# Kernel optimization log

Measured on AMD Instinct MI355X. Metric: run time of the kernel, lower is better.

The kernel has to match this reference:

```python
import jax, jax.numpy as jnp
import numpy as np

N, E = 100000, 1600000
HID, N_CHUNKS, STRU = 128, 8, 4


def setup_inputs() -> dict:
    key = jax.random.key(0)
    ks = jax.random.split(key, 7)
    x = jax.random.normal(ks[0], (N, HID), dtype=jnp.float32)
    e = jax.random.randint(ks[1], (2, E), 0, N, dtype=jnp.int64)
    ratio = jax.random.uniform(ks[2], (), dtype=jnp.float32)
    out_w = N_CHUNKS * STRU
    Wq = jax.random.normal(ks[3], (out_w, HID), dtype=jnp.float32) / np.sqrt(HID)
    bq = jax.random.normal(ks[4], (out_w,), dtype=jnp.float32) * 0.01
    Wv = jax.random.normal(ks[5], (out_w, HID), dtype=jnp.float32) / np.sqrt(HID)
    bv = jax.random.normal(ks[6], (out_w,), dtype=jnp.float32) * 0.01
    return {"x": x, "e": e, "ratio": ratio, "Wq": Wq, "bq": bq, "Wv": Wv, "bv": bv}


def reference(x, e, ratio, Wq, bq, Wv, bv):
    # edge-indexed gather of endpoint features: [E, HID]
    eu = x[e[0]]
    ev = x[e[1]]
    # two linear projections, elementwise multiply: [E, STRU*N_CHUNKS]
    ku = eu @ Wq.T + bq
    kv = ev @ Wv.T + bv
    ks = ku * kv
    # hsplit(STRU) -> STRU contiguous chunks of width N_CHUNKS; sum each chunk
    sums = ks.reshape(E, STRU, N_CHUNKS).sum(axis=-1)  # [E, STRU]
    w = jax.nn.sigmoid(sums) * (1.0 - ratio) * 0.5 + 1.0
    # original returns a list of STRU arrays of shape [E]; stack for a single output
    return jnp.transpose(w)  # [STRU, E]
```

## Files before the change

kernel.cpp:

```cpp
#include <hip/hip_runtime.h>
#include <hip/hip_bf16.h>
#include <cstddef>

constexpr int HID  = 128;
constexpr int OUTW = 32;
constexpr int TOT  = 64;
constexpr int STRU = 4;
constexpr int NCH  = 8;

typedef short  bf16x8 __attribute__((ext_vector_type(8)));
typedef float  f32x4  __attribute__((ext_vector_type(4)));
typedef int    int4v  __attribute__((ext_vector_type(4)));
typedef unsigned short u16x8 __attribute__((ext_vector_type(8)));

__device__ __forceinline__ unsigned short f2bf(float f) {
    unsigned u = __builtin_bit_cast(unsigned, f);
    u += 0x7FFFu + ((u >> 16) & 1u);
    return (unsigned short)(u >> 16);
}

__device__ __forceinline__ float dot4(float4 a, float4 b) {
    return a.x * b.x + a.y * b.y + a.z * b.z + a.w * b.w;
}

__device__ __forceinline__ float bfdot(int4v a, int4v b, float sum) {
#pragma unroll
    for (int w = 0; w < 4; ++w) {
        float alo = __builtin_bit_cast(float, (unsigned)(a[w] << 16));
        float ahi = __builtin_bit_cast(float, (unsigned)a[w] & 0xffff0000u);
        float blo = __builtin_bit_cast(float, (unsigned)(b[w] << 16));
        float bhi = __builtin_bit_cast(float, (unsigned)b[w] & 0xffff0000u);
        sum = fmaf(alo, blo, sum);
        sum = fmaf(ahi, bhi, sum);
    }
    return sum;
}

__global__ __launch_bounds__(256) void prep_bf16(
    const float* __restrict__ Wq, const float* __restrict__ bq,
    const float* __restrict__ Wv, const float* __restrict__ bv,
    unsigned short* __restrict__ Wfrag, float* __restrict__ bias)
{
    int tid = blockIdx.x * blockDim.x + threadIdx.x;
    if (tid < TOT * HID) {
        int j    = tid & 7;
        int lane = (tid >> 3) & 63;
        int kc   = (tid >> 9) & 3;
        int t    = tid >> 11;
        int o = t * 16 + (lane & 15);
        int k = kc * 32 + (lane >> 4) * 8 + j;
        float w = (o < OUTW) ? Wq[o * HID + k] : Wv[(o - OUTW) * HID + k];
        Wfrag[tid] = f2bf(w);
    }
    if (tid < TOT) bias[tid] = (tid < OUTW) ? bq[tid] : bv[tid - OUTW];
}

__global__ __launch_bounds__(256) void proj_mfma(
    const float* __restrict__ x,
    const unsigned short* __restrict__ Wfrag,
    const float* __restrict__ bias,
    unsigned short* __restrict__ P,
    unsigned short* __restrict__ Q,
    int n_nodes)
{
    __shared__ unsigned short sW[16 * 64 * 8];
    __shared__ unsigned short sPQ[64][TOT + 8];

    const int tid  = threadIdx.x;
    const int wid  = tid >> 6;
    const int lane = tid & 63;
    const int lr   = lane & 15;
    const int lg   = lane >> 4;
    const int base = blockIdx.x * 64;
    const int m0   = base + wid * 16;

    const int  arow = m0 + lr;
    const bool aok  = arow < n_nodes;
    const float* ap = x + (size_t)arow * HID;

    f32x4 xv[8];
#pragma unroll
    for (int kc = 0; kc < 4; ++kc) {
        if (aok) {
            const f32x4* p = reinterpret_cast<const f32x4*>(ap + kc * 32 + lg * 8);
            xv[2 * kc + 0] = p[0];
            xv[2 * kc + 1] = p[1];
        } else {
            xv[2 * kc + 0] = (f32x4)0.f;
            xv[2 * kc + 1] = (f32x4)0.f;
        }
    }

    {
        const int4v* src = reinterpret_cast<const int4v*>(Wfrag);
        int4v*       dst = reinterpret_cast<int4v*>(sW);
#pragma unroll
        for (int j = 0; j < 4; ++j)
            dst[tid + 256 * j] = src[tid + 256 * j];
    }

    f32x4 acc[4];
#pragma unroll
    for (int t = 0; t < 4; ++t) {
        float b = bias[t * 16 + lr];
        acc[t][0] = b; acc[t][1] = b; acc[t][2] = b; acc[t][3] = b;
    }

    __syncthreads();

#pragma unroll
    for (int kc = 0; kc < 4; ++kc) {
        f32x4 f0 = xv[2 * kc + 0], f1 = xv[2 * kc + 1];
        bf16x8 a;
        a[0] = (short)f2bf(f0[0]); a[1] = (short)f2bf(f0[1]);
        a[2] = (short)f2bf(f0[2]); a[3] = (short)f2bf(f0[3]);
        a[4] = (short)f2bf(f1[0]); a[5] = (short)f2bf(f1[1]);
        a[6] = (short)f2bf(f1[2]); a[7] = (short)f2bf(f1[3]);
#pragma unroll
        for (int t = 0; t < 4; ++t) {
            bf16x8 bf = *reinterpret_cast<const bf16x8*>(sW + ((size_t)(t * 4 + kc) * 64 + lane) * 8);
            acc[t] = __builtin_amdgcn_mfma_f32_16x16x32_bf16(a, bf, acc[t], 0, 0, 0);
        }
    }

    const int lrow = wid * 16 + lg * 4;
#pragma unroll
    for (int t = 0; t < 4; ++t)
#pragma unroll
        for (int j = 0; j < 4; ++j)
            sPQ[lrow + j][t * 16 + lr] = f2bf(acc[t][j]);
    __syncthreads();

    const int row  = tid >> 2;
    const int q    = tid & 3;
    const int node = base + row;
    if (node < n_nodes) {
        const int scol = q * 16;
        u16x8 v0 = *reinterpret_cast<const u16x8*>(&sPQ[row][scol]);
        u16x8 v1 = *reinterpret_cast<const u16x8*>(&sPQ[row][scol + 8]);
        unsigned short* dstbase = (q < 2) ? (P + (size_t)node * OUTW + q * 16)
                                          : (Q + (size_t)node * OUTW + (q - 2) * 16);
        u16x8* dst = reinterpret_cast<u16x8*>(dstbase);
        dst[0] = v0;
        dst[1] = v1;
    }
}

__global__ __launch_bounds__(256) void edge_bf16(
    const int* __restrict__ e,
    const unsigned short* __restrict__ P,
    const unsigned short* __restrict__ Q,
    const float* __restrict__ ratio_p,
    float* __restrict__ out, int E_)
{
    int i = blockIdx.x * blockDim.x + threadIdx.x;
    if (i >= E_) return;

    float scale = (1.0f - ratio_p[0]) * 0.5f;
    int e0 = __builtin_nontemporal_load(e + i);
    int e1 = __builtin_nontemporal_load(e + E_ + i);

    const int4v* p4 = reinterpret_cast<const int4v*>(P + (size_t)e0 * OUTW);
    const int4v* q4 = reinterpret_cast<const int4v*>(Q + (size_t)e1 * OUTW);

    int4v a[STRU], b[STRU];
#pragma unroll
    for (int s = 0; s < STRU; ++s) { a[s] = p4[s]; b[s] = q4[s]; }

#pragma unroll
    for (int s = 0; s < STRU; ++s) {
        float sum = bfdot(a[s], b[s], 0.f);
        float sig = 1.0f / (1.0f + __expf(-sum));
        float r   = sig * scale + 1.0f;
        __builtin_nontemporal_store(r, out + (size_t)s * E_ + i);
    }
}

__global__ __launch_bounds__(256) void fused_kernel(
    const float* __restrict__ x,
    const int* __restrict__ e,
    const float* __restrict__ ratio_p,
    const float* __restrict__ Wq, const float* __restrict__ bq,
    const float* __restrict__ Wv, const float* __restrict__ bv,
    float* __restrict__ out, int E_)
{
    int i = blockIdx.x * blockDim.x + threadIdx.x;
    if (i >= E_) return;

    float scale = (1.0f - ratio_p[0]) * 0.5f;
    int e0 = e[i];
    int e1 = e[E_ + i];

    const float4* __restrict__ xu  = reinterpret_cast<const float4*>(x + (size_t)e0 * HID);
    const float4* __restrict__ xv_ = reinterpret_cast<const float4*>(x + (size_t)e1 * HID);
    const float4* __restrict__ Wq4 = reinterpret_cast<const float4*>(Wq);
    const float4* __restrict__ Wv4 = reinterpret_cast<const float4*>(Wv);

#pragma unroll 1
    for (int s = 0; s < STRU; ++s) {
        float accP[NCH], accQ[NCH];
#pragma unroll
        for (int c = 0; c < NCH; ++c) { accP[c] = bq[s*NCH+c]; accQ[c] = bv[s*NCH+c]; }
        for (int kc = 0; kc < HID / 4; ++kc) {
            float4 u = xu[kc];
            float4 v = xv_[kc];
#pragma unroll
            for (int c = 0; c < NCH; ++c) {
                int o = s * NCH + c;
                accP[c] += dot4(u, Wq4[o * (HID / 4) + kc]);
                accQ[c] += dot4(v, Wv4[o * (HID / 4) + kc]);
            }
        }
        float sum = 0.0f;
#pragma unroll
        for (int c = 0; c < NCH; ++c) sum += accP[c] * accQ[c];
        float sig = 1.0f / (1.0f + __expf(-sum));
        out[(size_t)s * E_ + i] = sig * scale + 1.0f;
    }
}

extern "C" void kernel_launch(void* const* d_in, const int* in_sizes, int n_in,
                              void* d_out, int out_size, void* d_ws, size_t ws_size,
                              hipStream_t stream)
{
    const float* x     = (const float*)d_in[0];
    const int*   e     = (const int*)  d_in[1];
    const float* ratio = (const float*)d_in[2];
    const float* Wq    = (const float*)d_in[3];
    const float* bq    = (const float*)d_in[4];
    const float* Wv    = (const float*)d_in[5];
    const float* bv    = (const float*)d_in[6];
    float* out = (float*)d_out;

    int N_ = in_sizes[0] / HID;
    int E_ = in_sizes[1] / 2;

    size_t need = (size_t)N_ * OUTW * 2 * sizeof(unsigned short)
                + (size_t)TOT * HID * sizeof(unsigned short)
                + TOT * sizeof(float);
    if (ws_size >= need) {
        unsigned short* P     = (unsigned short*)d_ws;
        unsigned short* Qb    = P + (size_t)N_ * OUTW;
        unsigned short* Wfrag = Qb + (size_t)N_ * OUTW;
        float*          bias  = (float*)(Wfrag + (size_t)TOT * HID);

        prep_bf16<<<(TOT * HID + 255) / 256, 256, 0, stream>>>(Wq, bq, Wv, bv, Wfrag, bias);
        proj_mfma<<<(N_ + 63) / 64, 256, 0, stream>>>(x, Wfrag, bias, P, Qb, N_);
        edge_bf16<<<(E_ + 255) / 256, 256, 0, stream>>>(e, P, Qb, ratio, out, E_);
    } else {
        fused_kernel<<<(E_ + 255) / 256, 256, 0, stream>>>(x, e, ratio, Wq, bq, Wv, bv, out, E_);
    }
}
```

Before: 68.41 us.

## Fold weight prep into projection kernel and process two edges per thread

Drops the separate prep_bf16 launch: each projection block now reads Wq/Wv in fp32 directly, converts to bf16 and lays out MFMA fragments in shared memory, with the bias read straight from bq/bv. The edge kernel now handles two edges per thread (i and i+G) so more independent gathers are in flight per thread. This removes one kernel launch and its dependency, at the cost of redundant weight conversion in every projection block. The edge kernel also gains higher register use and uses half as many threads.

```diff
diff --git a/kernel.cpp b/kernel.cpp
--- a/kernel.cpp
+++ b/kernel.cpp
@@ -36,34 +36,15 @@
     return sum;
 }
 
-__global__ __launch_bounds__(256) void prep_bf16(
+__global__ __launch_bounds__(256) void proj_mfma(
+    const float* __restrict__ x,
     const float* __restrict__ Wq, const float* __restrict__ bq,
     const float* __restrict__ Wv, const float* __restrict__ bv,
-    unsigned short* __restrict__ Wfrag, float* __restrict__ bias)
-{
-    int tid = blockIdx.x * blockDim.x + threadIdx.x;
-    if (tid < TOT * HID) {
-        int j    = tid & 7;
-        int lane = (tid >> 3) & 63;
-        int kc   = (tid >> 9) & 3;
-        int t    = tid >> 11;
-        int o = t * 16 + (lane & 15);
-        int k = kc * 32 + (lane >> 4) * 8 + j;
-        float w = (o < OUTW) ? Wq[o * HID + k] : Wv[(o - OUTW) * HID + k];
-        Wfrag[tid] = f2bf(w);
-    }
-    if (tid < TOT) bias[tid] = (tid < OUTW) ? bq[tid] : bv[tid - OUTW];
-}
-
-__global__ __launch_bounds__(256) void proj_mfma(
-    const float* __restrict__ x,
-    const unsigned short* __restrict__ Wfrag,
-    const float* __restrict__ bias,
     unsigned short* __restrict__ P,
     unsigned short* __restrict__ Q,
     int n_nodes)
 {
-    __shared__ unsigned short sW[16 * 64 * 8];
+    __shared__ unsigned short sW[TOT * HID];
     __shared__ unsigned short sPQ[64][TOT + 8];
 
     const int tid  = threadIdx.x;
@@ -91,18 +72,28 @@
         }
     }
 
-    {
-        const int4v* src = reinterpret_cast<const int4v*>(Wfrag);
-        int4v*       dst = reinterpret_cast<int4v*>(sW);
-#pragma unroll
-        for (int j = 0; j < 4; ++j)
-            dst[tid + 256 * j] = src[tid + 256 * j];
+#pragma unroll
+    for (int g = 0; g < 4; ++g) {
+        int f     = tid * 8 + g * 2048;
+        int lane6 = (f >> 3) & 63;
+        int kc    = (f >> 9) & 3;
+        int t     = f >> 11;
+        int o     = t * 16 + (lane6 & 15);
+        int k0    = kc * 32 + (lane6 >> 4) * 8;
+        const float* wrow = (o < OUTW) ? (Wq + (size_t)o * HID)
+                                       : (Wv + (size_t)(o - OUTW) * HID);
+        f32x4 w0 = *reinterpret_cast<const f32x4*>(wrow + k0);
+        f32x4 w1 = *reinterpret_cast<const f32x4*>(wrow + k0 + 4);
+        u16x8 pk;
+        pk[0] = f2bf(w0[0]); pk[1] = f2bf(w0[1]); pk[2] = f2bf(w0[2]); pk[3] = f2bf(w0[3]);
+        pk[4] = f2bf(w1[0]); pk[5] = f2bf(w1[1]); pk[6] = f2bf(w1[2]); pk[7] = f2bf(w1[3]);
+        *reinterpret_cast<u16x8*>(sW + f) = pk;
     }
 
     f32x4 acc[4];
 #pragma unroll
     for (int t = 0; t < 4; ++t) {
-        float b = bias[t * 16 + lr];
+        float b = (t < 2) ? bq[t * 16 + lr] : bv[(t - 2) * 16 + lr];
         acc[t][0] = b; acc[t][1] = b; acc[t][2] = b; acc[t][3] = b;
     }
 
@@ -146,33 +137,49 @@
     }
 }
 
-__global__ __launch_bounds__(256) void edge_bf16(
+__global__ __launch_bounds__(256, 1) void edge_bf16_x2(
     const int* __restrict__ e,
     const unsigned short* __restrict__ P,
     const unsigned short* __restrict__ Q,
     const float* __restrict__ ratio_p,
-    float* __restrict__ out, int E_)
-{
-    int i = blockIdx.x * blockDim.x + threadIdx.x;
-    if (i >= E_) return;
+    float* __restrict__ out, int E_, int G)
+{
+    int i0 = blockIdx.x * blockDim.x + threadIdx.x;
+    if (i0 >= G) return;
+    int i1 = i0 + G;
+    const bool has2 = (i1 < E_);
 
     float scale = (1.0f - ratio_p[0]) * 0.5f;
-    int e0 = __builtin_nontemporal_load(e + i);
-    int e1 = __builtin_nontemporal_load(e + E_ + i);
-
-    const int4v* p4 = reinterpret_cast<const int4v*>(P + (size_t)e0 * OUTW);
-    const int4v* q4 = reinterpret_cast<const int4v*>(Q + (size_t)e1 * OUTW);
-
-    int4v a[STRU], b[STRU];
-#pragma unroll
-    for (int s = 0; s < STRU; ++s) { a[s] = p4[s]; b[s] = q4[s]; }
+
+    int e0a = __builtin_nontemporal_load(e + i0);
+    int e1a = __builtin_nontemporal_load(e + E_ + i0);
+    int e0b = e0a, e1b = e1a;
+    if (has2) {
+        e0b = __builtin_nontemporal_load(e + i1);
+        e1b = __builtin_nontemporal_load(e + E_ + i1);
+    }
+
+    const int4v* pA = reinterpret_cast<const int4v*>(P + (size_t)e0a * OUTW);
+    const int4v* qA = reinterpret_cast<const int4v*>(Q + (size_t)e1a * OUTW);
+    const int4v* pB = reinterpret_cast<const int4v*>(P + (size_t)e0b * OUTW);
+    const int4v* qB = reinterpret_cast<const int4v*>(Q + (size_t)e1b * OUTW);
+
+    int4v a0[STRU], b0[STRU], a1[STRU], b1[STRU];
+#pragma unroll
+    for (int s = 0; s < STRU; ++s) { a0[s] = pA[s]; b0[s] = qA[s]; }
+#pragma unroll
+    for (int s = 0; s < STRU; ++s) { a1[s] = pB[s]; b1[s] = qB[s]; }
 
 #pragma unroll
     for (int s = 0; s < STRU; ++s) {
-        float sum = bfdot(a[s], b[s], 0.f);
-        float sig = 1.0f / (1.0f + __expf(-sum));
-        float r   = sig * scale + 1.0f;
-        __builtin_nontemporal_store(r, out + (size_t)s * E_ + i);
+        float s0 = bfdot(a0[s], b0[s], 0.f);
+        float r0 = 1.0f / (1.0f + __expf(-s0)) * scale + 1.0f;
+        __builtin_nontemporal_store(r0, out + (size_t)s * E_ + i0);
+        if (has2) {
+            float s1 = bfdot(a1[s], b1[s], 0.f);
+            float r1 = 1.0f / (1.0f + __expf(-s1)) * scale + 1.0f;
+            __builtin_nontemporal_store(r1, out + (size_t)s * E_ + i1);
+        }
     }
 }
 
@@ -235,18 +242,14 @@
     int N_ = in_sizes[0] / HID;
     int E_ = in_sizes[1] / 2;
 
-    size_t need = (size_t)N_ * OUTW * 2 * sizeof(unsigned short)
-                + (size_t)TOT * HID * sizeof(unsigned short)
-                + TOT * sizeof(float);
+    size_t need = (size_t)N_ * OUTW * 2 * sizeof(unsigned short);
     if (ws_size >= need) {
-        unsigned short* P     = (unsigned short*)d_ws;
-        unsigned short* Qb    = P + (size_t)N_ * OUTW;
-        unsigned short* Wfrag = Qb + (size_t)N_ * OUTW;
-        float*          bias  = (float*)(Wfrag + (size_t)TOT * HID);
-
-        prep_bf16<<<(TOT * HID + 255) / 256, 256, 0, stream>>>(Wq, bq, Wv, bv, Wfrag, bias);
-        proj_mfma<<<(N_ + 63) / 64, 256, 0, stream>>>(x, Wfrag, bias, P, Qb, N_);
-        edge_bf16<<<(E_ + 255) / 256, 256, 0, stream>>>(e, P, Qb, ratio, out, E_);
+        unsigned short* P  = (unsigned short*)d_ws;
+        unsigned short* Qb = P + (size_t)N_ * OUTW;
+
+        proj_mfma<<<(N_ + 63) / 64, 256, 0, stream>>>(x, Wq, bq, Wv, bv, P, Qb, N_);
+        int G = (E_ + 1) / 2;
+        edge_bf16_x2<<<(G + 255) / 256, 256, 0, stream>>>(e, P, Qb, ratio, out, E_, G);
     } else {
         fused_kernel<<<(E_ + 255) / 256, 256, 0, stream>>>(x, e, ratio, Wq, bq, Wv, bv, out, E_);
     }
```

Measured after the change: 78.41 us. 14.6% more time.
